# Optimization experiments

Measured on AMD Instinct MI355X. Metric: run time of the kernel, lower is better.

Reference implementation:

```python
import jax, jax.numpy as jnp
import numpy as np

N = 131072        # active input voxels (= output voxels for submanifold conv)
KVOL = 27         # 3x3x3 kernel volume
P = 65536         # neighbor pairs per kernel offset (regularized kernel map)
CIN = 64
COUT = 64


def setup_inputs() -> dict:
    key = jax.random.key(0)
    k1, k2, k3, k4, k5 = jax.random.split(key, 5)
    in_feats = jax.random.normal(k1, (N, CIN), dtype=jnp.float32)
    kernel = jax.random.normal(k2, (KVOL, CIN, COUT), dtype=jnp.float32) * (1.0 / np.sqrt(CIN * KVOL))
    bias_param = jax.random.normal(k3, (COUT,), dtype=jnp.float32)
    imap = jax.random.randint(k4, (KVOL, P), 0, N, dtype=jnp.int32)
    omap = jax.random.randint(k5, (KVOL, P), 0, N, dtype=jnp.int32)
    return {"in_feats": in_feats, "kernel": kernel, "bias_param": bias_param,
            "imap": imap, "omap": omap}


def reference(in_feats, kernel, bias_param, imap, omap):
    # Sparse 3D conv as gather -> per-offset GEMM -> scatter-add.
    # gathered: [KVOL, P, CIN]
    gathered = in_feats[imap]
    # per-offset GEMM: [KVOL, P, COUT]
    contrib = jnp.einsum('kpc,kco->kpo', gathered, kernel)
    out = jnp.zeros((N, COUT), dtype=in_feats.dtype)
    out = out.at[omap.reshape(-1)].add(contrib.reshape(-1, COUT))
    out = out + bias_param
    return out
```

## Files before the change

### kernel.cpp

```cpp
#include <hip/hip_runtime.h>
#include <hip/hip_bf16.h>
#include <stdint.h>

#define N_VOX 131072
#define KVOL  27
#define PPK   65536
#define CIN   64
#define COUT  64
#define TOT   (KVOL * PPK)
#define RANK_BLOCKS 864

typedef __attribute__((ext_vector_type(8))) short short8;
typedef __attribute__((ext_vector_type(4))) float f32x4;

__device__ __forceinline__ void gl_lds16(const void* g, void* l) {
  __builtin_amdgcn_global_load_lds(
      (const __attribute__((address_space(1))) unsigned int*)g,
      (__attribute__((address_space(3))) unsigned int*)l,
      16, 0, 0);
}

__device__ __forceinline__ unsigned short f2bf(float f) {
  __hip_bfloat16 h = __float2bfloat16(f);
  return *reinterpret_cast<unsigned short*>(&h);
}


__global__ __launch_bounds__(256) void prep_rank_kernel(
    const float* __restrict__ in, unsigned short* __restrict__ inb,
    const float* __restrict__ w, unsigned short* __restrict__ wt,
    const int* __restrict__ omap, int* __restrict__ cnt, int* __restrict__ rank,
    int do_rank) {
  int b = blockIdx.x;
  if (b < 4096) {
    int i = b * 256 + threadIdx.x;
    const float4* in4 = (const float4*)in;
    float4 f0 = in4[2 * i], f1 = in4[2 * i + 1];
    union { unsigned short u[8]; short8 v; } r;
    r.u[0] = f2bf(f0.x); r.u[1] = f2bf(f0.y); r.u[2] = f2bf(f0.z); r.u[3] = f2bf(f0.w);
    r.u[4] = f2bf(f1.x); r.u[5] = f2bf(f1.y); r.u[6] = f2bf(f1.z); r.u[7] = f2bf(f1.w);
    ((short8*)inb)[i] = r.v;
  } else if (b < 4096 + KVOL) {
    int k = b - 4096;
    const float* wk = w + k * CIN * COUT;
    unsigned short* wtk = wt + k * CIN * COUT;
    for (int idx = threadIdx.x; idx < CIN * COUT; idx += 256) {
      int c = idx >> 6, o = idx & 63;
      wtk[o * 64 + c] = f2bf(wk[idx]);
    }
  } else if (do_rank) {
    int e0 = ((b - 4096 - KVOL) * 256 + threadIdx.x) * 8;
    int4 o0 = *(const int4*)(omap + e0);
    int4 o1 = *(const int4*)(omap + e0 + 4);
    int r0, r1, r2, r3, r4, r5, r6, r7;
    r0 = atomicAdd(&cnt[o0.x], 1);
    r1 = atomicAdd(&cnt[o0.y], 1);
    r2 = atomicAdd(&cnt[o0.z], 1);
    r3 = atomicAdd(&cnt[o0.w], 1);
    r4 = atomicAdd(&cnt[o1.x], 1);
    r5 = atomicAdd(&cnt[o1.y], 1);
    r6 = atomicAdd(&cnt[o1.z], 1);
    r7 = atomicAdd(&cnt[o1.w], 1);
    *(int4*)(rank + e0)     = make_int4(r0, r1, r2, r3);
    *(int4*)(rank + e0 + 4) = make_int4(r4, r5, r6, r7);
  }
}

__global__ __launch_bounds__(256) void scan_kernel(const int* __restrict__ cnt,
                                                   int* __restrict__ ofs,
                                                   int* __restrict__ gctr) {
  __shared__ int s[256];
  __shared__ int base_s;
  int i = blockIdx.x * 256 + threadIdx.x;
  int v = cnt[i];
  s[threadIdx.x] = v; __syncthreads();
  for (int off = 1; off < 256; off <<= 1) {
    int t = (threadIdx.x >= off) ? s[threadIdx.x - off] : 0;
    __syncthreads();
    s[threadIdx.x] += t;
    __syncthreads();
  }
  if (threadIdx.x == 255) base_s = atomicAdd(gctr, s[255]);
  __syncthreads();
  ofs[i] = base_s + s[threadIdx.x] - v;
}


__global__ __launch_bounds__(256) void spconv_store_kernel(
    const unsigned short* __restrict__ inb,
    const unsigned short* __restrict__ wt,
    const int* __restrict__ imap,
    const int* __restrict__ omap,
    const int* __restrict__ rank,
    const int* __restrict__ ofs,
    unsigned short* __restrict__ contrib) {
  __shared__ __align__(16) char smem[24576];
  short* A_lds = (short*)smem;
  short* B_lds = (short*)(smem + 16384);
  short* C_sh  = (short*)smem;
  __shared__ int perm_s[128];

  int bid = blockIdx.x;
  int k = bid >> 9;
  int pbase = (bid & 511) * 128;
  int tid = threadIdx.x;
  int wave = tid >> 6, lane = tid & 63;
  int m = lane & 15, q = lane >> 4;

  const int* imk = imap + k * PPK;
  const unsigned short* wtk = wt + k * 4096;

  if (tid < 128) {
    int e = k * PPK + pbase + tid;
    perm_s[tid] = rank[e] + ofs[omap[e]];
  }

#pragma unroll
  for (int i = 0; i < 2; i++) {
    int id = wave * 2 + i;
    int t = id >> 1, s = id & 1;
    const unsigned short* g = wtk + (t * 16 + m) * 64 + s * 32 + q * 8;
    gl_lds16(g, &B_lds[(t * 128 + s * 64) * 8]);
  }
#pragma unroll
  for (int j = 0; j < 2; j++) {
    int r = wave * 2 + j;
    int row = imk[pbase + r * 16 + m];
    const unsigned short* g0 = inb + row * 64 + q * 8;
    gl_lds16(g0,      &A_lds[(r * 128)      * 8]);
    gl_lds16(g0 + 32, &A_lds[(r * 128 + 64) * 8]);
  }
  __syncthreads();

  const short8* Af = (const short8*)A_lds;
  const short8* Bf = (const short8*)B_lds;

  short8 a[2][2], b[4][2];
#pragma unroll
  for (int r2 = 0; r2 < 2; r2++) {
    int r = wave * 2 + r2;
#pragma unroll
    for (int s = 0; s < 2; s++) a[r2][s] = Af[r * 128 + s * 64 + lane];
  }
#pragma unroll
  for (int t = 0; t < 4; t++)
#pragma unroll
    for (int s = 0; s < 2; s++) b[t][s] = Bf[t * 128 + s * 64 + lane];

  __syncthreads();

  f32x4 acc[2][4];
#pragma unroll
  for (int r2 = 0; r2 < 2; r2++)
#pragma unroll
    for (int t = 0; t < 4; t++) {
      f32x4 c = {0.f, 0.f, 0.f, 0.f};
      c = __builtin_amdgcn_mfma_f32_16x16x32_bf16(a[r2][0], b[t][0], c, 0, 0, 0);
      c = __builtin_amdgcn_mfma_f32_16x16x32_bf16(a[r2][1], b[t][1], c, 0, 0, 0);
      acc[r2][t] = c;
    }

#pragma unroll
  for (int r2 = 0; r2 < 2; r2++) {
    int pl = (wave * 2 + r2) * 16 + q * 4;
#pragma unroll
    for (int t = 0; t < 4; t++)
#pragma unroll
      for (int reg = 0; reg < 4; reg++)
        C_sh[(pl + reg) * 72 + t * 16 + m] = (short)f2bf(acc[r2][t][reg]);
  }
  __syncthreads();

#pragma unroll
  for (int i = 0; i < 4; i++) {
    int id = i * 256 + tid;
    int row = id >> 3, ch = (id & 7) * 8;
    short8 v = *(const short8*)&C_sh[row * 72 + ch];
    __builtin_nontemporal_store(v, (short8*)&contrib[(size_t)perm_s[row] * 64 + ch]);
  }
}


__global__ __launch_bounds__(256) void reduce_kernel(
    const unsigned short* __restrict__ contrib,
    const int* __restrict__ ofs,
    const int* __restrict__ cnt,
    const float* __restrict__ bias,
    float* __restrict__ out) {
  int row = blockIdx.x * 4 + (threadIdx.x >> 6);
  int lane = threadIdx.x & 63;
  int rg = lane >> 3, ch = (lane & 7) * 8;
  int s = ofs[row], n = cnt[row];

  float acc[8];
#pragma unroll
  for (int i = 0; i < 8; i++) acc[i] = 0.f;

  int j = rg;
  for (; j + 8 < n; j += 16) {
    short8 v0 = __builtin_nontemporal_load((const short8*)&contrib[(size_t)(s + j) * 64 + ch]);
    short8 v1 = __builtin_nontemporal_load((const short8*)&contrib[(size_t)(s + j + 8) * 64 + ch]);
#pragma unroll
    for (int i = 0; i < 8; i++)
      acc[i] += __uint_as_float((unsigned int)(unsigned short)v0[i] << 16);
#pragma unroll
    for (int i = 0; i < 8; i++)
      acc[i] += __uint_as_float((unsigned int)(unsigned short)v1[i] << 16);
  }
  if (j < n) {
    short8 v0 = __builtin_nontemporal_load((const short8*)&contrib[(size_t)(s + j) * 64 + ch]);
#pragma unroll
    for (int i = 0; i < 8; i++)
      acc[i] += __uint_as_float((unsigned int)(unsigned short)v0[i] << 16);
  }

#pragma unroll
  for (int mask = 8; mask < 64; mask <<= 1)
#pragma unroll
    for (int i = 0; i < 8; i++) acc[i] += __shfl_xor(acc[i], mask, 64);

  if (rg == 0) {
    float4 b0 = *(const float4*)(bias + ch);
    float4 b1 = *(const float4*)(bias + ch + 4);
    float4 r0 = {acc[0] + b0.x, acc[1] + b0.y, acc[2] + b0.z, acc[3] + b0.w};
    float4 r1 = {acc[4] + b1.x, acc[5] + b1.y, acc[6] + b1.z, acc[7] + b1.w};
    *(float4*)(out + (size_t)row * 64 + ch) = r0;
    *(float4*)(out + (size_t)row * 64 + ch + 4) = r1;
  }
}


__global__ __launch_bounds__(256) void init_out_kernel(float* __restrict__ out,
                                                       const float* __restrict__ bias) {
  int i = blockIdx.x * blockDim.x + threadIdx.x;
  float4 b = *(const float4*)(bias + ((i * 4) & 63));
  ((float4*)out)[i] = b;
}

__global__ __launch_bounds__(256) void spconv_atomic_kernel(
    const unsigned short* __restrict__ inb,
    const unsigned short* __restrict__ wt,
    const int* __restrict__ imap, const int* __restrict__ omap,
    float* __restrict__ out) {
  __shared__ __align__(16) short A_lds[128 * 64];
  __shared__ __align__(16) short B_lds[64 * 64];

  int bid = blockIdx.x;
  int k = bid >> 9;
  int pbase = (bid & 511) * 128;
  int tid = threadIdx.x;
  int wave = tid >> 6, lane = tid & 63;
  int m = lane & 15, q = lane >> 4;

  const int* imk = imap + k * PPK;
  const int* omk = omap + k * PPK;
  const unsigned short* wtk = wt + k * 4096;

#pragma unroll
  for (int i = 0; i < 2; i++) {
    int id = wave * 2 + i;
    int t = id >> 1, s = id & 1;
    const unsigned short* g = wtk + (t * 16 + m) * 64 + s * 32 + q * 8;
    gl_lds16(g, &B_lds[(t * 128 + s * 64) * 8]);
  }
#pragma unroll
  for (int j = 0; j < 2; j++) {
    int r = wave * 2 + j;
    int row = imk[pbase + r * 16 + m];
    const unsigned short* g0 = inb + row * 64 + q * 8;
    gl_lds16(g0,      &A_lds[(r * 128)      * 8]);
    gl_lds16(g0 + 32, &A_lds[(r * 128 + 64) * 8]);
  }
  __syncthreads();

  const short8* Af = (const short8*)A_lds;
  const short8* Bf = (const short8*)B_lds;
  short8 a[2][2], b[4][2];
#pragma unroll
  for (int r2 = 0; r2 < 2; r2++) {
    int r = wave * 2 + r2;
#pragma unroll
    for (int s = 0; s < 2; s++) a[r2][s] = Af[r * 128 + s * 64 + lane];
  }
#pragma unroll
  for (int t = 0; t < 4; t++)
#pragma unroll
    for (int s = 0; s < 2; s++) b[t][s] = Bf[t * 128 + s * 64 + lane];

  f32x4 acc[2][4];
#pragma unroll
  for (int r2 = 0; r2 < 2; r2++)
#pragma unroll
    for (int t = 0; t < 4; t++) {
      f32x4 c = {0.f, 0.f, 0.f, 0.f};
      c = __builtin_amdgcn_mfma_f32_16x16x32_bf16(a[r2][0], b[t][0], c, 0, 0, 0);
      c = __builtin_amdgcn_mfma_f32_16x16x32_bf16(a[r2][1], b[t][1], c, 0, 0, 0);
      acc[r2][t] = c;
    }

  int orow[2][4];
#pragma unroll
  for (int r2 = 0; r2 < 2; r2++) {
    int pr = pbase + (wave * 2 + r2) * 16 + q * 4;
#pragma unroll
    for (int reg = 0; reg < 4; reg++) orow[r2][reg] = omk[pr + reg];
  }
#pragma unroll
  for (int r2 = 0; r2 < 2; r2++)
#pragma unroll
    for (int t = 0; t < 4; t++)
#pragma unroll
      for (int reg = 0; reg < 4; reg++)
        atomicAdd(out + (size_t)orow[r2][reg] * 64 + t * 16 + m, acc[r2][t][reg]);
}


extern "C" void kernel_launch(void* const* d_in, const int* in_sizes, int n_in,
                              void* d_out, int out_size, void* d_ws, size_t ws_size,
                              hipStream_t stream) {
  const float* in_feats = (const float*)d_in[0];
  const float* kern     = (const float*)d_in[1];
  const float* bias     = (const float*)d_in[2];
  const int*   imap     = (const int*)d_in[3];
  const int*   omap     = (const int*)d_in[4];
  float* out = (float*)d_out;

  char* ws = (char*)d_ws;
  size_t off = 0;
  auto alloc = [&](size_t bytes) { size_t o = off; off = (off + bytes + 255) & ~(size_t)255; return o; };

  size_t o_inb  = alloc((size_t)N_VOX * CIN * 2);
  size_t o_wt   = alloc((size_t)KVOL * CIN * COUT * 2);
  size_t o_cnt  = alloc((size_t)(N_VOX + 1) * 4);
  size_t o_ofs  = alloc((size_t)N_VOX * 4);
  size_t o_rank = alloc((size_t)TOT * 4);
  size_t o_ctb  = alloc((size_t)TOT * 64 * 2);
  size_t needed = off;

  unsigned short* inb = (unsigned short*)(ws + o_inb);
  unsigned short* wt  = (unsigned short*)(ws + o_wt);
  int* cnt  = (int*)(ws + o_cnt);
  int* gctr = cnt + N_VOX;
  int* ofs  = (int*)(ws + o_ofs);
  int* rank = (int*)(ws + o_rank);
  unsigned short* ctb = (unsigned short*)(ws + o_ctb);

  bool fast = (ws_size >= needed);

  if (fast) {
    (void)hipMemsetAsync(cnt, 0, (size_t)(N_VOX + 1) * 4, stream);
    prep_rank_kernel<<<4096 + KVOL + RANK_BLOCKS, 256, 0, stream>>>(
        in_feats, inb, kern, wt, omap, cnt, rank, 1);
    scan_kernel<<<N_VOX / 256, 256, 0, stream>>>(cnt, ofs, gctr);
    spconv_store_kernel<<<KVOL * (PPK / 128), 256, 0, stream>>>(
        inb, wt, imap, omap, rank, ofs, ctb);
    reduce_kernel<<<N_VOX / 4, 256, 0, stream>>>(ctb, ofs, cnt, bias, out);
  } else {
    prep_rank_kernel<<<4096 + KVOL, 256, 0, stream>>>(
        in_feats, inb, kern, wt, omap, nullptr, nullptr, 0);
    init_out_kernel<<<(N_VOX * COUT / 4) / 256, 256, 0, stream>>>(out, bias);
    spconv_atomic_kernel<<<KVOL * (PPK / 128), 256, 0, stream>>>(inb, wt, imap, omap, out);
  }
}
```

Before: 303.6 us.

## Fuse rank counting into GEMM launch and gather via permutation in reduce

```diff
diff --git a/kernel.cpp b/kernel.cpp
--- a/kernel.cpp
+++ b/kernel.cpp
@@ -9,6 +9,7 @@
 #define COUT  64
 #define TOT   (KVOL * PPK)
 #define RANK_BLOCKS 864
+#define GEMM_BLOCKS (KVOL * (PPK / 128))
 
 typedef __attribute__((ext_vector_type(8))) short short8;
 typedef __attribute__((ext_vector_type(4))) float f32x4;
@@ -26,11 +27,9 @@
 }
 
 
-__global__ __launch_bounds__(256) void prep_rank_kernel(
+__global__ __launch_bounds__(256) void prep_kernel(
     const float* __restrict__ in, unsigned short* __restrict__ inb,
-    const float* __restrict__ w, unsigned short* __restrict__ wt,
-    const int* __restrict__ omap, int* __restrict__ cnt, int* __restrict__ rank,
-    int do_rank) {
+    const float* __restrict__ w, unsigned short* __restrict__ wt) {
   int b = blockIdx.x;
   if (b < 4096) {
     int i = b * 256 + threadIdx.x;
@@ -40,7 +39,7 @@
     r.u[0] = f2bf(f0.x); r.u[1] = f2bf(f0.y); r.u[2] = f2bf(f0.z); r.u[3] = f2bf(f0.w);
     r.u[4] = f2bf(f1.x); r.u[5] = f2bf(f1.y); r.u[6] = f2bf(f1.z); r.u[7] = f2bf(f1.w);
     ((short8*)inb)[i] = r.v;
-  } else if (b < 4096 + KVOL) {
+  } else {
     int k = b - 4096;
     const float* wk = w + k * CIN * COUT;
     unsigned short* wtk = wt + k * CIN * COUT;
@@ -48,8 +47,19 @@
       int c = idx >> 6, o = idx & 63;
       wtk[o * 64 + c] = f2bf(wk[idx]);
     }
-  } else if (do_rank) {
-    int e0 = ((b - 4096 - KVOL) * 256 + threadIdx.x) * 8;
+  }
+}
+
+
+__global__ __launch_bounds__(256) void gemm_rank_kernel(
+    const unsigned short* __restrict__ inb,
+    const unsigned short* __restrict__ wt,
+    const int* __restrict__ imap,
+    const int* __restrict__ omap,
+    int* __restrict__ cnt, int* __restrict__ rank,
+    unsigned short* __restrict__ contrib) {
+  if (blockIdx.x < RANK_BLOCKS) {
+    int e0 = (blockIdx.x * 256 + threadIdx.x) * 8;
     int4 o0 = *(const int4*)(omap + e0);
     int4 o1 = *(const int4*)(omap + e0 + 4);
     int r0, r1, r2, r3, r4, r5, r6, r7;
@@ -63,6 +73,87 @@
     r7 = atomicAdd(&cnt[o1.w], 1);
     *(int4*)(rank + e0)     = make_int4(r0, r1, r2, r3);
     *(int4*)(rank + e0 + 4) = make_int4(r4, r5, r6, r7);
+    return;
+  }
+
+  __shared__ __align__(16) char smem[24576];
+  short* A_lds = (short*)smem;
+  short* B_lds = (short*)(smem + 16384);
+  short* C_sh  = (short*)smem;
+
+  int bid = blockIdx.x - RANK_BLOCKS;
+  int k = bid >> 9;
+  int pbase = (bid & 511) * 128;
+  int tid = threadIdx.x;
+  int wave = tid >> 6, lane = tid & 63;
+  int m = lane & 15, q = lane >> 4;
+
+  const int* imk = imap + k * PPK;
+  const unsigned short* wtk = wt + k * 4096;
+  size_t ebase = (size_t)k * PPK + pbase;
+
+#pragma unroll
+  for (int i = 0; i < 2; i++) {
+    int id = wave * 2 + i;
+    int t = id >> 1, s = id & 1;
+    const unsigned short* g = wtk + (t * 16 + m) * 64 + s * 32 + q * 8;
+    gl_lds16(g, &B_lds[(t * 128 + s * 64) * 8]);
+  }
+#pragma unroll
+  for (int j = 0; j < 2; j++) {
+    int r = wave * 2 + j;
+    int row = imk[pbase + r * 16 + m];
+    const unsigned short* g0 = inb + row * 64 + q * 8;
+    gl_lds16(g0,      &A_lds[(r * 128)      * 8]);
+    gl_lds16(g0 + 32, &A_lds[(r * 128 + 64) * 8]);
+  }
+  __syncthreads();
+
+  const short8* Af = (const short8*)A_lds;
+  const short8* Bf = (const short8*)B_lds;
+
+  short8 a[2][2], b[4][2];
+#pragma unroll
+  for (int r2 = 0; r2 < 2; r2++) {
+    int r = wave * 2 + r2;
+#pragma unroll
+    for (int s = 0; s < 2; s++) a[r2][s] = Af[r * 128 + s * 64 + lane];
+  }
+#pragma unroll
+  for (int t = 0; t < 4; t++)
+#pragma unroll
+    for (int s = 0; s < 2; s++) b[t][s] = Bf[t * 128 + s * 64 + lane];
+
+  __syncthreads();
+
+  f32x4 acc[2][4];
+#pragma unroll
+  for (int r2 = 0; r2 < 2; r2++)
+#pragma unroll
+    for (int t = 0; t < 4; t++) {
+      f32x4 c = {0.f, 0.f, 0.f, 0.f};
+      c = __builtin_amdgcn_mfma_f32_16x16x32_bf16(a[r2][0], b[t][0], c, 0, 0, 0);
+      c = __builtin_amdgcn_mfma_f32_16x16x32_bf16(a[r2][1], b[t][1], c, 0, 0, 0);
+      acc[r2][t] = c;
+    }
+
+#pragma unroll
+  for (int r2 = 0; r2 < 2; r2++) {
+    int pl = (wave * 2 + r2) * 16 + q * 4;
+#pragma unroll
+    for (int t = 0; t < 4; t++)
+#pragma unroll
+      for (int reg = 0; reg < 4; reg++)
+        C_sh[(pl + reg) * 72 + t * 16 + m] = (short)f2bf(acc[r2][t][reg]);
+  }
+  __syncthreads();
+
+#pragma unroll
+  for (int i = 0; i < 4; i++) {
+    int id = i * 256 + tid;
+    int row = id >> 3, ch = (id & 7) * 8;
+    short8 v = *(const short8*)&C_sh[row * 72 + ch];
+    __builtin_nontemporal_store(v, (short8*)&contrib[(ebase + row) * 64 + ch]);
   }
 }
 
@@ -85,104 +176,28 @@
   ofs[i] = base_s + s[threadIdx.x] - v;
 }
 
-
-__global__ __launch_bounds__(256) void spconv_store_kernel(
-    const unsigned short* __restrict__ inb,
-    const unsigned short* __restrict__ wt,
-    const int* __restrict__ imap,
-    const int* __restrict__ omap,
-    const int* __restrict__ rank,
-    const int* __restrict__ ofs,
-    unsigned short* __restrict__ contrib) {
-  __shared__ __align__(16) char smem[24576];
-  short* A_lds = (short*)smem;
-  short* B_lds = (short*)(smem + 16384);
-  short* C_sh  = (short*)smem;
-  __shared__ int perm_s[128];
-
-  int bid = blockIdx.x;
-  int k = bid >> 9;
-  int pbase = (bid & 511) * 128;
-  int tid = threadIdx.x;
-  int wave = tid >> 6, lane = tid & 63;
-  int m = lane & 15, q = lane >> 4;
-
-  const int* imk = imap + k * PPK;
-  const unsigned short* wtk = wt + k * 4096;
-
-  if (tid < 128) {
-    int e = k * PPK + pbase + tid;
-    perm_s[tid] = rank[e] + ofs[omap[e]];
-  }
-
-#pragma unroll
-  for (int i = 0; i < 2; i++) {
-    int id = wave * 2 + i;
-    int t = id >> 1, s = id & 1;
-    const unsigned short* g = wtk + (t * 16 + m) * 64 + s * 32 + q * 8;
-    gl_lds16(g, &B_lds[(t * 128 + s * 64) * 8]);
-  }
-#pragma unroll
-  for (int j = 0; j < 2; j++) {
-    int r = wave * 2 + j;
-    int row = imk[pbase + r * 16 + m];
-    const unsigned short* g0 = inb + row * 64 + q * 8;
-    gl_lds16(g0,      &A_lds[(r * 128)      * 8]);
-    gl_lds16(g0 + 32, &A_lds[(r * 128 + 64) * 8]);
-  }
-  __syncthreads();
-
-  const short8* Af = (const short8*)A_lds;
-  const short8* Bf = (const short8*)B_lds;
-
-  short8 a[2][2], b[4][2];
-#pragma unroll
-  for (int r2 = 0; r2 < 2; r2++) {
-    int r = wave * 2 + r2;
-#pragma unroll
-    for (int s = 0; s < 2; s++) a[r2][s] = Af[r * 128 + s * 64 + lane];
-  }
-#pragma unroll
-  for (int t = 0; t < 4; t++)
-#pragma unroll
-    for (int s = 0; s < 2; s++) b[t][s] = Bf[t * 128 + s * 64 + lane];
-
-  __syncthreads();
-
-  f32x4 acc[2][4];
-#pragma unroll
-  for (int r2 = 0; r2 < 2; r2++)
-#pragma unroll
-    for (int t = 0; t < 4; t++) {
-      f32x4 c = {0.f, 0.f, 0.f, 0.f};
-      c = __builtin_amdgcn_mfma_f32_16x16x32_bf16(a[r2][0], b[t][0], c, 0, 0, 0);
-      c = __builtin_amdgcn_mfma_f32_16x16x32_bf16(a[r2][1], b[t][1], c, 0, 0, 0);
-      acc[r2][t] = c;
-    }
-
-#pragma unroll
-  for (int r2 = 0; r2 < 2; r2++) {
-    int pl = (wave * 2 + r2) * 16 + q * 4;
-#pragma unroll
-    for (int t = 0; t < 4; t++)
-#pragma unroll
-      for (int reg = 0; reg < 4; reg++)
-        C_sh[(pl + reg) * 72 + t * 16 + m] = (short)f2bf(acc[r2][t][reg]);
-  }
-  __syncthreads();
-
-#pragma unroll
-  for (int i = 0; i < 4; i++) {
-    int id = i * 256 + tid;
-    int row = id >> 3, ch = (id & 7) * 8;
-    short8 v = *(const short8*)&C_sh[row * 72 + ch];
-    __builtin_nontemporal_store(v, (short8*)&contrib[(size_t)perm_s[row] * 64 + ch]);
-  }
+__global__ __launch_bounds__(256) void scatter_kernel(
+    const int* __restrict__ omap, const int* __restrict__ rank,
+    const int* __restrict__ ofs, int* __restrict__ perm) {
+  int e0 = (blockIdx.x * 256 + threadIdx.x) * 8;
+  int4 o0 = *(const int4*)(omap + e0);
+  int4 o1 = *(const int4*)(omap + e0 + 4);
+  int4 r0 = *(const int4*)(rank + e0);
+  int4 r1 = *(const int4*)(rank + e0 + 4);
+  perm[ofs[o0.x] + r0.x] = e0;
+  perm[ofs[o0.y] + r0.y] = e0 + 1;
+  perm[ofs[o0.z] + r0.z] = e0 + 2;
+  perm[ofs[o0.w] + r0.w] = e0 + 3;
+  perm[ofs[o1.x] + r1.x] = e0 + 4;
+  perm[ofs[o1.y] + r1.y] = e0 + 5;
+  perm[ofs[o1.z] + r1.z] = e0 + 6;
+  perm[ofs[o1.w] + r1.w] = e0 + 7;
 }
 
 
 __global__ __launch_bounds__(256) void reduce_kernel(
     const unsigned short* __restrict__ contrib,
+    const int* __restrict__ perm,
     const int* __restrict__ ofs,
     const int* __restrict__ cnt,
     const float* __restrict__ bias,
@@ -198,8 +213,10 @@
 
   int j = rg;
   for (; j + 8 < n; j += 16) {
-    short8 v0 = __builtin_nontemporal_load((const short8*)&contrib[(size_t)(s + j) * 64 + ch]);
-    short8 v1 = __builtin_nontemporal_load((const short8*)&contrib[(size_t)(s + j + 8) * 64 + ch]);
+    size_t i0 = (size_t)perm[s + j];
+    size_t i1 = (size_t)perm[s + j + 8];
+    short8 v0 = __builtin_nontemporal_load((const short8*)&contrib[i0 * 64 + ch]);
+    short8 v1 = __builtin_nontemporal_load((const short8*)&contrib[i1 * 64 + ch]);
 #pragma unroll
     for (int i = 0; i < 8; i++)
       acc[i] += __uint_as_float((unsigned int)(unsigned short)v0[i] << 16);
@@ -208,7 +225,8 @@
       acc[i] += __uint_as_float((unsigned int)(unsigned short)v1[i] << 16);
   }
   if (j < n) {
-    short8 v0 = __builtin_nontemporal_load((const short8*)&contrib[(size_t)(s + j) * 64 + ch]);
+    size_t i0 = (size_t)perm[s + j];
+    short8 v0 = __builtin_nontemporal_load((const short8*)&contrib[i0 * 64 + ch]);
 #pragma unroll
     for (int i = 0; i < 8; i++)
       acc[i] += __uint_as_float((unsigned int)(unsigned short)v0[i] << 16);
@@ -344,21 +362,21 @@
   int* ofs  = (int*)(ws + o_ofs);
   int* rank = (int*)(ws + o_rank);
   unsigned short* ctb = (unsigned short*)(ws + o_ctb);
+  int* perm = (int*)(ws + o_inb);
 
   bool fast = (ws_size >= needed);
 
   if (fast) {
     (void)hipMemsetAsync(cnt, 0, (size_t)(N_VOX + 1) * 4, stream);
-    prep_rank_kernel<<<4096 + KVOL + RANK_BLOCKS, 256, 0, stream>>>(
-        in_feats, inb, kern, wt, omap, cnt, rank, 1);
+    prep_kernel<<<4096 + KVOL, 256, 0, stream>>>(in_feats, inb, kern, wt);
+    gemm_rank_kernel<<<RANK_BLOCKS + GEMM_BLOCKS, 256, 0, stream>>>(
+        inb, wt, imap, omap, cnt, rank, ctb);
     scan_kernel<<<N_VOX / 256, 256, 0, stream>>>(cnt, ofs, gctr);
-    spconv_store_kernel<<<KVOL * (PPK / 128), 256, 0, stream>>>(
-        inb, wt, imap, omap, rank, ofs, ctb);
-    reduce_kernel<<<N_VOX / 4, 256, 0, stream>>>(ctb, ofs, cnt, bias, out);
+    scatter_kernel<<<RANK_BLOCKS, 256, 0, stream>>>(omap, rank, ofs, perm);
+    reduce_kernel<<<N_VOX / 4, 256, 0, stream>>>(ctb, perm, ofs, cnt, bias, out);
   } else {
-    prep_rank_kernel<<<4096 + KVOL, 256, 0, stream>>>(
-        in_feats, inb, kern, wt, omap, nullptr, nullptr, 0);
+    prep_kernel<<<4096 + KVOL, 256, 0, stream>>>(in_feats, inb, kern, wt);
     init_out_kernel<<<(N_VOX * COUT / 4) / 256, 256, 0, stream>>>(out, bias);
-    spconv_atomic_kernel<<<KVOL * (PPK / 128), 256, 0, stream>>>(inb, wt, imap, omap, out);
-  }
-}
+    spconv_atomic_kernel<<<GEMM_BLOCKS, 256, 0, stream>>>(inb, wt, imap, omap, out);
+  }
+}
```

Measured after the change: 339.8 us. 11.9% more time.

## Replace global atomic ranking and scan with two-pass bucketed counting sort

Applied to the files above, without the earlier changes.

```diff
diff --git a/kernel.cpp b/kernel.cpp
--- a/kernel.cpp
+++ b/kernel.cpp
@@ -8,7 +8,11 @@
 #define CIN   64
 #define COUT  64
 #define TOT   (KVOL * PPK)
-#define RANK_BLOCKS 864
+#define SORT_BLOCKS 864
+#define GEMM_BLOCKS (KVOL * (PPK / 128))
+#define NBUCKET 256
+#define BUCKET_CAP 8192
+#define CURSOR_STRIDE 16
 
 typedef __attribute__((ext_vector_type(8))) short short8;
 typedef __attribute__((ext_vector_type(4))) float f32x4;
@@ -26,12 +30,44 @@
 }
 
 
-__global__ __launch_bounds__(256) void prep_rank_kernel(
+__global__ __launch_bounds__(256) void prep_sort1_kernel(
     const float* __restrict__ in, unsigned short* __restrict__ inb,
     const float* __restrict__ w, unsigned short* __restrict__ wt,
-    const int* __restrict__ omap, int* __restrict__ cnt, int* __restrict__ rank,
-    int do_rank) {
+    const int* __restrict__ omap, unsigned int* __restrict__ cursor,
+    unsigned int* __restrict__ pairs, int do_sort) {
   int b = blockIdx.x;
+  if (do_sort) {
+    if (b < SORT_BLOCKS) {
+      __shared__ unsigned int hist[NBUCKET];
+      __shared__ unsigned int bbase[NBUCKET];
+      int tid = threadIdx.x;
+      hist[tid] = 0;
+      __syncthreads();
+      int e0 = (b * 256 + tid) * 8;
+      int4 o0 = *(const int4*)(omap + e0);
+      int4 o1 = *(const int4*)(omap + e0 + 4);
+      unsigned int k[8] = {(unsigned)o0.x, (unsigned)o0.y, (unsigned)o0.z, (unsigned)o0.w,
+                           (unsigned)o1.x, (unsigned)o1.y, (unsigned)o1.z, (unsigned)o1.w};
+#pragma unroll
+      for (int i = 0; i < 8; i++) atomicAdd(&hist[k[i] >> 9], 1u);
+      __syncthreads();
+      unsigned int n = hist[tid];
+      unsigned int base = n ? atomicAdd(&cursor[tid * CURSOR_STRIDE], n) : 0u;
+      bbase[tid] = (unsigned)tid * BUCKET_CAP + base;
+      hist[tid] = 0;
+      __syncthreads();
+#pragma unroll
+      for (int i = 0; i < 8; i++) {
+        unsigned int bk = k[i] >> 9;
+        unsigned int r = atomicAdd(&hist[bk], 1u);
+        unsigned int pos = bbase[bk] + r;
+        if (pos < (bk + 1) * BUCKET_CAP)
+          pairs[pos] = (((unsigned)(e0 + i)) << 9) | (k[i] & 511u);
+      }
+      return;
+    }
+    b -= SORT_BLOCKS;
+  }
   if (b < 4096) {
     int i = b * 256 + threadIdx.x;
     const float4* in4 = (const float4*)in;
@@ -40,7 +76,7 @@
     r.u[0] = f2bf(f0.x); r.u[1] = f2bf(f0.y); r.u[2] = f2bf(f0.z); r.u[3] = f2bf(f0.w);
     r.u[4] = f2bf(f1.x); r.u[5] = f2bf(f1.y); r.u[6] = f2bf(f1.z); r.u[7] = f2bf(f1.w);
     ((short8*)inb)[i] = r.v;
-  } else if (b < 4096 + KVOL) {
+  } else {
     int k = b - 4096;
     const float* wk = w + k * CIN * COUT;
     unsigned short* wtk = wt + k * CIN * COUT;
@@ -48,41 +84,61 @@
       int c = idx >> 6, o = idx & 63;
       wtk[o * 64 + c] = f2bf(wk[idx]);
     }
-  } else if (do_rank) {
-    int e0 = ((b - 4096 - KVOL) * 256 + threadIdx.x) * 8;
-    int4 o0 = *(const int4*)(omap + e0);
-    int4 o1 = *(const int4*)(omap + e0 + 4);
-    int r0, r1, r2, r3, r4, r5, r6, r7;
-    r0 = atomicAdd(&cnt[o0.x], 1);
-    r1 = atomicAdd(&cnt[o0.y], 1);
-    r2 = atomicAdd(&cnt[o0.z], 1);
-    r3 = atomicAdd(&cnt[o0.w], 1);
-    r4 = atomicAdd(&cnt[o1.x], 1);
-    r5 = atomicAdd(&cnt[o1.y], 1);
-    r6 = atomicAdd(&cnt[o1.z], 1);
-    r7 = atomicAdd(&cnt[o1.w], 1);
-    *(int4*)(rank + e0)     = make_int4(r0, r1, r2, r3);
-    *(int4*)(rank + e0 + 4) = make_int4(r4, r5, r6, r7);
-  }
-}
-
-__global__ __launch_bounds__(256) void scan_kernel(const int* __restrict__ cnt,
-                                                   int* __restrict__ ofs,
-                                                   int* __restrict__ gctr) {
-  __shared__ int s[256];
-  __shared__ int base_s;
-  int i = blockIdx.x * 256 + threadIdx.x;
-  int v = cnt[i];
-  s[threadIdx.x] = v; __syncthreads();
-  for (int off = 1; off < 256; off <<= 1) {
-    int t = (threadIdx.x >= off) ? s[threadIdx.x - off] : 0;
+  }
+}
+
+
+__global__ __launch_bounds__(512) void sort_pass2_kernel(
+    const unsigned int* __restrict__ cursor, const unsigned int* __restrict__ pairs,
+    int* __restrict__ islot, int* __restrict__ ofs, int* __restrict__ cnt) {
+  __shared__ unsigned int hist[512];
+  __shared__ unsigned int binofs[512];
+  __shared__ unsigned int csc[512];
+  __shared__ unsigned int sb_s, n_s;
+  int b = blockIdx.x, tid = threadIdx.x;
+
+  unsigned int cv = (tid < NBUCKET) ? cursor[tid * CURSOR_STRIDE] : 0u;
+  csc[tid] = cv;
+  __syncthreads();
+  for (int off = 1; off < 512; off <<= 1) {
+    unsigned int t = (tid >= off) ? csc[tid - off] : 0u;
     __syncthreads();
-    s[threadIdx.x] += t;
+    csc[tid] += t;
     __syncthreads();
   }
-  if (threadIdx.x == 255) base_s = atomicAdd(gctr, s[255]);
-  __syncthreads();
-  ofs[i] = base_s + s[threadIdx.x] - v;
+  if (tid == b) {
+    sb_s = csc[tid] - cv;
+    n_s  = cv > BUCKET_CAP ? BUCKET_CAP : cv;
+  }
+  hist[tid] = 0;
+  __syncthreads();
+  unsigned int sb = sb_s, n = n_s;
+  const unsigned int* reg = pairs + (size_t)b * BUCKET_CAP;
+
+  for (unsigned int i = tid; i < n; i += 512)
+    atomicAdd(&hist[reg[i] & 511u], 1u);
+  __syncthreads();
+
+  unsigned int h = hist[tid];
+  csc[tid] = h;
+  __syncthreads();
+  for (int off = 1; off < 512; off <<= 1) {
+    unsigned int t = (tid >= off) ? csc[tid - off] : 0u;
+    __syncthreads();
+    csc[tid] += t;
+    __syncthreads();
+  }
+  binofs[tid] = csc[tid] - h;
+  int key = (b << 9) | tid;
+  ofs[key] = (int)(sb + binofs[tid]);
+  cnt[key] = (int)h;
+  __syncthreads();
+
+  for (unsigned int i = tid; i < n; i += 512) {
+    unsigned int v = reg[i];
+    unsigned int r = atomicAdd(&binofs[v & 511u], 1u);
+    islot[v >> 9] = (int)(sb + r);
+  }
 }
 
 
@@ -90,9 +146,7 @@
     const unsigned short* __restrict__ inb,
     const unsigned short* __restrict__ wt,
     const int* __restrict__ imap,
-    const int* __restrict__ omap,
-    const int* __restrict__ rank,
-    const int* __restrict__ ofs,
+    const int* __restrict__ islot,
     unsigned short* __restrict__ contrib) {
   __shared__ __align__(16) char smem[24576];
   short* A_lds = (short*)smem;
@@ -110,10 +164,7 @@
   const int* imk = imap + k * PPK;
   const unsigned short* wtk = wt + k * 4096;
 
-  if (tid < 128) {
-    int e = k * PPK + pbase + tid;
-    perm_s[tid] = rank[e] + ofs[omap[e]];
-  }
+  if (tid < 128) perm_s[tid] = islot[k * PPK + pbase + tid];
 
 #pragma unroll
   for (int i = 0; i < 2; i++) {
@@ -329,36 +380,37 @@
   size_t off = 0;
   auto alloc = [&](size_t bytes) { size_t o = off; off = (off + bytes + 255) & ~(size_t)255; return o; };
 
-  size_t o_inb  = alloc((size_t)N_VOX * CIN * 2);
-  size_t o_wt   = alloc((size_t)KVOL * CIN * COUT * 2);
-  size_t o_cnt  = alloc((size_t)(N_VOX + 1) * 4);
-  size_t o_ofs  = alloc((size_t)N_VOX * 4);
-  size_t o_rank = alloc((size_t)TOT * 4);
-  size_t o_ctb  = alloc((size_t)TOT * 64 * 2);
+  size_t o_inb   = alloc((size_t)N_VOX * CIN * 2);
+  size_t o_wt    = alloc((size_t)KVOL * CIN * COUT * 2);
+  size_t o_cnt   = alloc((size_t)N_VOX * 4);
+  size_t o_ofs   = alloc((size_t)N_VOX * 4);
+  size_t o_islot = alloc((size_t)TOT * 4);
+  size_t o_cur   = alloc((size_t)NBUCKET * CURSOR_STRIDE * 4);
+  size_t o_ctb   = alloc((size_t)TOT * 64 * 2);
   size_t needed = off;
 
   unsigned short* inb = (unsigned short*)(ws + o_inb);
   unsigned short* wt  = (unsigned short*)(ws + o_wt);
-  int* cnt  = (int*)(ws + o_cnt);
-  int* gctr = cnt + N_VOX;
-  int* ofs  = (int*)(ws + o_ofs);
-  int* rank = (int*)(ws + o_rank);
+  int* cnt   = (int*)(ws + o_cnt);
+  int* ofs   = (int*)(ws + o_ofs);
+  int* islot = (int*)(ws + o_islot);
+  unsigned int* cursor = (unsigned int*)(ws + o_cur);
   unsigned short* ctb = (unsigned short*)(ws + o_ctb);
+  unsigned int* pairs = (unsigned int*)(ws + o_ctb);
 
   bool fast = (ws_size >= needed);
 
   if (fast) {
-    (void)hipMemsetAsync(cnt, 0, (size_t)(N_VOX + 1) * 4, stream);
-    prep_rank_kernel<<<4096 + KVOL + RANK_BLOCKS, 256, 0, stream>>>(
-        in_feats, inb, kern, wt, omap, cnt, rank, 1);
-    scan_kernel<<<N_VOX / 256, 256, 0, stream>>>(cnt, ofs, gctr);
-    spconv_store_kernel<<<KVOL * (PPK / 128), 256, 0, stream>>>(
-        inb, wt, imap, omap, rank, ofs, ctb);
+    (void)hipMemsetAsync(cursor, 0, (size_t)NBUCKET * CURSOR_STRIDE * 4, stream);
+    prep_sort1_kernel<<<SORT_BLOCKS + 4096 + KVOL, 256, 0, stream>>>(
+        in_feats, inb, kern, wt, omap, cursor, pairs, 1);
+    sort_pass2_kernel<<<NBUCKET, 512, 0, stream>>>(cursor, pairs, islot, ofs, cnt);
+    spconv_store_kernel<<<GEMM_BLOCKS, 256, 0, stream>>>(inb, wt, imap, islot, ctb);
     reduce_kernel<<<N_VOX / 4, 256, 0, stream>>>(ctb, ofs, cnt, bias, out);
   } else {
-    prep_rank_kernel<<<4096 + KVOL, 256, 0, stream>>>(
+    prep_sort1_kernel<<<4096 + KVOL, 256, 0, stream>>>(
         in_feats, inb, kern, wt, omap, nullptr, nullptr, 0);
     init_out_kernel<<<(N_VOX * COUT / 4) / 256, 256, 0, stream>>>(out, bias);
-    spconv_atomic_kernel<<<KVOL * (PPK / 128), 256, 0, stream>>>(inb, wt, imap, omap, out);
-  }
-}
+    spconv_atomic_kernel<<<GEMM_BLOCKS, 256, 0, stream>>>(inb, wt, imap, omap, out);
+  }
+}
```

Result: faster. 262.2 us (-13.6%).
